# Optimization experiments

Measured on AMD Instinct MI355X. Metric: run time of the kernel, lower is better.

## Reference

```python
import jax, jax.numpy as jnp
import numpy as np

EPS = 1e-5  # torch.nn.CosineSimilarity eps


def setup_inputs() -> dict:
    key = jax.random.key(0)
    x = jax.random.normal(key, (8, 256, 1024), dtype=jnp.float32)
    return {"batch_sequence_tensors": x}


def _worst_sim(x):
    # For every contiguous window [s, e] (1 <= s < e <= S-1, matching
    # exclude_special_tokens + sequential combinatorics), compute
    # min_t in [s,e] cos(mean(x[s:e+1]), x[t]).
    # Trick: dot(sum_{s..e} x_i, x_t) comes from a prefix sum of the Gram
    # matrix, and ||sum_{s..e} x||^2 from a 2-D prefix sum of the Gram matrix,
    # avoiding any [B,S,S,D] intermediates.
    B, S, D = x.shape
    G = jnp.einsum('bsd,btd->bst', x, x)  # [B,S,S] Gram

    # num[b,s,e,t] = sum_{i=s..e} x_i . x_t  via 1-D prefix sum over i
    Cpad = jnp.pad(jnp.cumsum(G, axis=1), ((0, 0), (1, 0), (0, 0)))  # [B,S+1,S]
    num = Cpad[:, 1:, :][:, None, :, :] - Cpad[:, :S, :][:, :, None, :]  # [B,S,S,S]

    # ||sum_{s..e} x||^2 = sum_{i,j in [s,e]} G[i,j] via 2-D prefix sum
    PP = jnp.pad(jnp.cumsum(jnp.cumsum(G, axis=1), axis=2),
                 ((0, 0), (1, 0), (1, 0)))  # [B,S+1,S+1]
    dE = jnp.diagonal(PP[:, 1:, 1:], axis1=1, axis2=2)   # PP[e+1,e+1]  [B,S]
    dS = jnp.diagonal(PP[:, :S, :S], axis1=1, axis2=2)   # PP[s,s]      [B,S]
    cross1 = PP[:, :S, 1:]                               # PP[s,e+1]  axes (s,e)
    cross2 = jnp.swapaxes(PP[:, 1:, :S], 1, 2)           # PP[e+1,s] -> (s,e)
    ssq = dE[:, None, :] + dS[:, :, None] - cross1 - cross2  # [B,S,S]
    sum_norm = jnp.sqrt(jnp.maximum(ssq, 0.0))               # ||sum||

    idx = jnp.arange(S)
    win_len = jnp.maximum(idx[None, :] - idx[:, None] + 1, 1).astype(x.dtype)  # [S,S] (s,e)
    # center = sum / len ; cosine uses the mean exactly as the torch module
    mean_norm = sum_norm / win_len                       # [B,S,S]
    x_norm = jnp.sqrt(jnp.maximum(jnp.diagonal(G, axis1=1, axis2=2), 0.0))  # [B,S]
    denom = jnp.maximum(mean_norm[..., None] * x_norm[:, None, None, :], EPS)
    cos = (num / win_len[None, :, :, None]) / denom      # [B,S,S,S]

    t_in = (idx[None, None, :] >= idx[:, None, None]) & \
           (idx[None, None, :] <= idx[None, :, None])    # [S,S,S] (s,e,t)
    worst = jnp.min(jnp.where(t_in[None], cos, jnp.inf), axis=-1)  # [B,S,S]

    valid = (idx[:, None] >= 1) & (idx[None, :] > idx[:, None])    # 1<=s<e<=S-1
    return jnp.where(valid[None], worst, 0.0)


def reference(batch_sequence_tensors):
    # worst_sim[b,s,e] = min cosine similarity of window mean vs members;
    # the original module's group mask is worst_sim >= threshold (0.9),
    # followed by (data-dependent, non-tensor) subset removal.
    return _worst_sim(batch_sequence_tensors)
```

## Files before the change

kernel.cpp:

```cpp
#include <hip/hip_runtime.h>
#include <stdint.h>

#define NB 8
#define NS 256
#define ND 1024
#define EPSF 1e-5f
#define BIGF 3.0e38f

typedef __attribute__((ext_vector_type(8))) short short8;
typedef __attribute__((ext_vector_type(4))) float f32x4;

__device__ __forceinline__ unsigned short f2bf(float f) {
  unsigned int u = __float_as_uint(f);
  u = (u + 0x7FFFu + ((u >> 16) & 1u)) >> 16;
  return (unsigned short)u;
}
__device__ __forceinline__ float bf2f(unsigned short u) {
  return __uint_as_float((unsigned int)u << 16);
}

__global__ __launch_bounds__(256) void k_convert(const float* __restrict__ x,
                                                 unsigned short* __restrict__ xb,
                                                 float* __restrict__ DGa,
                                                 float* __restrict__ IXa) {
  int row = blockIdx.x * 4 + (threadIdx.x >> 6);
  int lane = threadIdx.x & 63;
  size_t base = (size_t)row * ND;
  float sq = 0.f;
#pragma unroll
  for (int c = 0; c < 4; ++c) {
    size_t o = base + c * 256 + lane * 4;
    float4 v = *reinterpret_cast<const float4*>(x + o);
    ushort4 ob;
    ob.x = f2bf(v.x); ob.y = f2bf(v.y); ob.z = f2bf(v.z); ob.w = f2bf(v.w);
    *reinterpret_cast<ushort4*>(xb + o) = ob;
    sq += v.x * v.x + v.y * v.y + v.z * v.z + v.w * v.w;
  }
#pragma unroll
  for (int off = 32; off; off >>= 1) sq += __shfl_xor(sq, off);
  if (lane == 0) {
    DGa[row] = sq;
    IXa[row] = 1.0f / sqrtf(sq);
  }
}

__global__ __launch_bounds__(256) void k_ypfx(const unsigned short* __restrict__ xb,
                                              unsigned short* __restrict__ yb) {
  int wid = (blockIdx.x * 256 + threadIdx.x) >> 6;
  int lane = threadIdx.x & 63;
  int b = wid >> 10;
  int d = wid & 1023;
  const unsigned short* xr = xb + ((size_t)b << 18) + d;
  unsigned short* yr = yb + ((size_t)b << 18) + d;
  int s0 = lane << 2;
  float v0 = bf2f(xr[(size_t)(s0 + 0) * ND]);
  float v1 = bf2f(xr[(size_t)(s0 + 1) * ND]);
  float v2 = bf2f(xr[(size_t)(s0 + 2) * ND]);
  float v3 = bf2f(xr[(size_t)(s0 + 3) * ND]);
  float sum = v0 + v1 + v2 + v3;
  float sc = sum;
#pragma unroll
  for (int off = 1; off < 64; off <<= 1) {
    float n = __shfl_up(sc, off);
    if (lane >= off) sc += n;
  }
  float y0 = (sc - sum) + v0;
  float y1 = y0 + v1;
  float y2 = y1 + v2;
  float y3 = y2 + v3;
  yr[(size_t)(s0 + 0) * ND] = f2bf(y0);
  yr[(size_t)(s0 + 1) * ND] = f2bf(y1);
  yr[(size_t)(s0 + 2) * ND] = f2bf(y2);
  yr[(size_t)(s0 + 3) * ND] = f2bf(y3);
}

__global__ __launch_bounds__(256) void k_gemmC(const unsigned short* __restrict__ yb,
                                               const unsigned short* __restrict__ xb,
                                               float* __restrict__ cp) {
  int gw = ((blockIdx.x << 8) + threadIdx.x) >> 6;
  int lane = threadIdx.x & 63;
  int b  = gw & 7;
  int mt = (gw >> 3) & 7;
  int nt = (gw >> 6) & 7;
  int ks = (gw >> 9) & 1;
  const unsigned short* Ab = yb + ((size_t)b << 18) + ((size_t)(mt << 5) << 10);
  const unsigned short* Bb = xb + ((size_t)b << 18) + ((size_t)(nt << 5) << 10);
  int lr = lane & 15;
  int lk = (lane >> 4) << 3;
  f32x4 acc00 = {0.f,0.f,0.f,0.f}, acc01 = {0.f,0.f,0.f,0.f};
  f32x4 acc10 = {0.f,0.f,0.f,0.f}, acc11 = {0.f,0.f,0.f,0.f};
  int kbase = (ks << 9) + lk;
#pragma unroll 2
  for (int kk = 0; kk < 512; kk += 32) {
    int ko = kbase + kk;
    short8 a0  = *reinterpret_cast<const short8*>(Ab + ((size_t)lr << 10) + ko);
    short8 a1  = *reinterpret_cast<const short8*>(Ab + ((size_t)(16 + lr) << 10) + ko);
    short8 bb0 = *reinterpret_cast<const short8*>(Bb + ((size_t)lr << 10) + ko);
    short8 bb1 = *reinterpret_cast<const short8*>(Bb + ((size_t)(16 + lr) << 10) + ko);
    acc00 = __builtin_amdgcn_mfma_f32_16x16x32_bf16(a0, bb0, acc00, 0, 0, 0);
    acc01 = __builtin_amdgcn_mfma_f32_16x16x32_bf16(a0, bb1, acc01, 0, 0, 0);
    acc10 = __builtin_amdgcn_mfma_f32_16x16x32_bf16(a1, bb0, acc10, 0, 0, 0);
    acc11 = __builtin_amdgcn_mfma_f32_16x16x32_bf16(a1, bb1, acc11, 0, 0, 0);
  }
  float* G = cp + (size_t)ks * (NB * NS * NS) + ((size_t)b << 16);
  int r0 = (mt << 5) + ((lane >> 4) << 2);
  int c0 = (nt << 5) + lr;
#pragma unroll
  for (int j = 0; j < 4; ++j) {
    G[(r0 + j) * NS + c0]           = acc00[j];
    G[(r0 + j) * NS + c0 + 16]      = acc01[j];
    G[(r0 + 16 + j) * NS + c0]      = acc10[j];
    G[(r0 + 16 + j) * NS + c0 + 16] = acc11[j];
  }
}

__global__ __launch_bounds__(256) void k_scan(const float* __restrict__ cp,
                                              float* __restrict__ C, float* __restrict__ S2) {
  int id = blockIdx.x * 4 + (threadIdx.x >> 6);
  int lane = threadIdx.x & 63;
  int b = id / 257;
  int r = id - b * 257;
  float* Crow = C + ((size_t)b * 257 + r) * NS;
  float* Srow = S2 + ((size_t)b * 257 + r) * 257;
  const float* p0 = cp + (((size_t)b << 8) + (r - 1)) * NS;
  const float* p1 = p0 + (size_t)NB * NS * NS;
  if (lane == 0) Srow[0] = 0.f;
  float run = 0.f;
  for (int c0 = 0; c0 < NS; c0 += 64) {
    float v = 0.f;
    if (r > 0) v = p0[c0 + lane] + p1[c0 + lane];
    Crow[c0 + lane] = v;
#pragma unroll
    for (int off = 1; off < 64; off <<= 1) {
      float n = __shfl_up(v, off);
      if (lane >= off) v += n;
    }
    Srow[c0 + lane + 1] = run + v;
    run += __shfl(v, 63);
  }
}

__global__ __launch_bounds__(256) void k_trop(const float* __restrict__ C,
                                              const float* __restrict__ S2,
                                              const float* __restrict__ IXa,
                                              const float* __restrict__ DGa,
                                              float* __restrict__ out) {
  __shared__ float As[64][36];
  __shared__ float Bs[64][68];
  __shared__ float wred[4];
  int blk = blockIdx.x;
  int b = blk >> 5;
  int tix = blk & 31;
  int i0 = (tix >> 2) << 5;
  int j0 = (tix & 3) << 6;
  int tid = threadIdx.x;
  float* outb = out + ((size_t)b << 16);

  if (i0 >= j0 + 63) {
    float4 z = {0.f, 0.f, 0.f, 0.f};
    float* p = outb + (size_t)(i0 + (tid >> 3)) * NS + j0 + ((tid & 7) << 3);
    reinterpret_cast<float4*>(p)[0] = z;
    reinterpret_cast<float4*>(p)[1] = z;
    return;
  }

  const float* Cb = C + (size_t)b * 257 * NS;
  const float* IXb = IXa + b * NS;

  float wv0 = IXb[tid];
#pragma unroll
  for (int off = 32; off; off >>= 1) wv0 = fmaxf(wv0, __shfl_xor(wv0, off));
  if ((tid & 63) == 0) wred[tid >> 6] = wv0;
  __syncthreads();
  float wmb = fmaxf(fmaxf(wred[0], wred[1]), fmaxf(wred[2], wred[3]));

  int ii0 = (tid >> 4) << 1;
  int jj0 = (tid & 15) << 2;
  float acc[8];
#pragma unroll
  for (int k = 0; k < 8; ++k) acc[k] = BIGF;

  int rA = tid >> 4;
  int c4 = (tid & 15) << 2;

  for (int t0 = i0 & ~63; t0 < j0 + 64; t0 += 64) {
    __syncthreads();
    float4 wv = *reinterpret_cast<const float4*>(IXb + t0 + c4);
#pragma unroll
    for (int p = 0; p < 2; ++p) {
      int r = i0 + p * 16 + rA;
      float4 v = *reinterpret_cast<const float4*>(Cb + (size_t)r * NS + t0 + c4);
      As[c4 + 0][p * 16 + rA] = v.x * wv.x;
      As[c4 + 1][p * 16 + rA] = v.y * wv.y;
      As[c4 + 2][p * 16 + rA] = v.z * wv.z;
      As[c4 + 3][p * 16 + rA] = v.w * wv.w;
    }
#pragma unroll
    for (int p = 0; p < 4; ++p) {
      int r = j0 + 1 + p * 16 + rA;
      float4 v = *reinterpret_cast<const float4*>(Cb + (size_t)r * NS + t0 + c4);
      Bs[c4 + 0][p * 16 + rA] = v.x * wv.x;
      Bs[c4 + 1][p * 16 + rA] = v.y * wv.y;
      Bs[c4 + 2][p * 16 + rA] = v.z * wv.z;
      Bs[c4 + 3][p * 16 + rA] = v.w * wv.w;
    }
    __syncthreads();

    int thA = i0 + ii0 - t0;
    int thB = j0 + jj0 - t0;
    if (thA <= -1 && thB >= 63) {
#pragma unroll 4
      for (int tt = 0; tt < 64; ++tt) {
        float2 a = *reinterpret_cast<const float2*>(&As[tt][ii0]);
        float4 bv = *reinterpret_cast<const float4*>(&Bs[tt][jj0]);
        acc[0] = fminf(acc[0], bv.x - a.x);
        acc[1] = fminf(acc[1], bv.y - a.x);
        acc[2] = fminf(acc[2], bv.z - a.x);
        acc[3] = fminf(acc[3], bv.w - a.x);
        acc[4] = fminf(acc[4], bv.x - a.y);
        acc[5] = fminf(acc[5], bv.y - a.y);
        acc[6] = fminf(acc[6], bv.z - a.y);
        acc[7] = fminf(acc[7], bv.w - a.y);
      }
    } else {
#pragma unroll 4
      for (int tt = 0; tt < 64; ++tt) {
        float2 a = *reinterpret_cast<const float2*>(&As[tt][ii0]);
        float4 bv = *reinterpret_cast<const float4*>(&Bs[tt][jj0]);
        float a0 = (tt >= thA)     ? a.x  : -BIGF;
        float a1 = (tt >= thA + 1) ? a.y  : -BIGF;
        float b0 = (tt <= thB)     ? bv.x :  BIGF;
        float b1 = (tt <= thB + 1) ? bv.y :  BIGF;
        float b2 = (tt <= thB + 2) ? bv.z :  BIGF;
        float b3 = (tt <= thB + 3) ? bv.w :  BIGF;
        acc[0] = fminf(acc[0], b0 - a0);
        acc[1] = fminf(acc[1], b1 - a0);
        acc[2] = fminf(acc[2], b2 - a0);
        acc[3] = fminf(acc[3], b3 - a0);
        acc[4] = fminf(acc[4], b0 - a1);
        acc[5] = fminf(acc[5], b1 - a1);
        acc[6] = fminf(acc[6], b2 - a1);
        acc[7] = fminf(acc[7], b3 - a1);
      }
    }
  }

  const float* S2b = S2 + (size_t)b * 257 * 257;
  const float* DGb = DGa + b * NS;
#pragma unroll
  for (int k = 0; k < 2; ++k) {
    int i = i0 + ii0 + k;
    float o4[4];
    float s2ii = S2b[(size_t)i * 257 + i];
#pragma unroll
    for (int l = 0; l < 4; ++l) {
      int j = j0 + jj0 + l;
      float res = 0.f;
      if (i >= 1 && j > i) {
        float s2jj = S2b[(size_t)(j + 1) * 257 + (j + 1)];
        float s2ij = S2b[(size_t)i * 257 + (j + 1)];
        float s2ji = S2b[(size_t)(j + 1) * 257 + i];
        float ssq = (s2jj - s2ij) - (s2ji - s2ii);
        float sn = sqrtf(fmaxf(ssq, 0.f));
        float win = (float)(j - i + 1);
        if (sn >= EPSF * win * wmb) {
          res = acc[k * 4 + l] / sn;
        } else {
          float mn = sn / win;
          float m = BIGF;
          const float* r2 = Cb + (size_t)(j + 1) * NS;
          const float* r1 = Cb + (size_t)i * NS;
          for (int t = i; t <= j; ++t) {
            float num = r2[t] - r1[t];
            float xn = sqrtf(fmaxf(DGb[t], 0.f));
            float den = fmaxf(mn * xn, EPSF);
            m = fminf(m, num / win / den);
          }
          res = m;
        }
      }
      o4[l] = res;
    }
    float4 st = {o4[0], o4[1], o4[2], o4[3]};
    *reinterpret_cast<float4*>(outb + (size_t)i * NS + j0 + jj0) = st;
  }
}

extern "C" void kernel_launch(void* const* d_in, const int* in_sizes, int n_in,
                              void* d_out, int out_size, void* d_ws, size_t ws_size,
                              hipStream_t stream) {
  (void)in_sizes; (void)n_in; (void)ws_size; (void)out_size;
  const float* x = (const float*)d_in[0];
  float* out = (float*)d_out;
  char* ws = (char*)d_ws;
  unsigned short* Xb = (unsigned short*)(ws);
  unsigned short* Yb = (unsigned short*)(ws + 4194304);
  float* Cp  = (float*)(ws + 8388608);
  float* C   = (float*)(ws + 12582912);
  float* S2  = (float*)(ws + 14688256);
  float* DGa = (float*)(ws + 16801824);
  float* IXa = (float*)(ws + 16810016);

  k_convert<<<512, 256, 0, stream>>>(x, Xb, DGa, IXa);
  k_ypfx<<<2048, 256, 0, stream>>>(Xb, Yb);
  k_gemmC<<<256, 256, 0, stream>>>(Yb, Xb, Cp);
  k_scan<<<514, 256, 0, stream>>>(Cp, C, S2);
  k_trop<<<256, 256, 0, stream>>>(C, S2, IXa, DGa, out);
}
```

Measured before the change: 120.9 us.

## Fuse all five stages into one cooperative kernel with grid syncs

Replaces the five kernel launches (convert, prefix, GEMM, scan, tropical min) with a single cooperative kernel of 256 blocks that separates the stages with grid.sync(). The prefix stage now reads fp32 x directly, so it no longer waits on the bf16 conversion. The GEMM drops the split-K partial buffer: each wave computes full-K 16x16 tiles and writes C directly, which removes the partial-sum add from the scan. The aim is to cut launch overhead and intermediate traffic, at the cost of grid-wide barriers and lower occupancy during the GEMM and scan phases.

```diff
diff --git a/kernel.cpp b/kernel.cpp
--- a/kernel.cpp
+++ b/kernel.cpp
@@ -1,5 +1,8 @@
 #include <hip/hip_runtime.h>
+#include <hip/hip_cooperative_groups.h>
 #include <stdint.h>
+
+namespace cg = cooperative_groups;
 
 #define NB 8
 #define NS 256
@@ -15,274 +18,267 @@
   u = (u + 0x7FFFu + ((u >> 16) & 1u)) >> 16;
   return (unsigned short)u;
 }
-__device__ __forceinline__ float bf2f(unsigned short u) {
-  return __uint_as_float((unsigned int)u << 16);
-}
-
-__global__ __launch_bounds__(256) void k_convert(const float* __restrict__ x,
-                                                 unsigned short* __restrict__ xb,
-                                                 float* __restrict__ DGa,
-                                                 float* __restrict__ IXa) {
-  int row = blockIdx.x * 4 + (threadIdx.x >> 6);
-  int lane = threadIdx.x & 63;
-  size_t base = (size_t)row * ND;
-  float sq = 0.f;
-#pragma unroll
-  for (int c = 0; c < 4; ++c) {
-    size_t o = base + c * 256 + lane * 4;
-    float4 v = *reinterpret_cast<const float4*>(x + o);
-    ushort4 ob;
-    ob.x = f2bf(v.x); ob.y = f2bf(v.y); ob.z = f2bf(v.z); ob.w = f2bf(v.w);
-    *reinterpret_cast<ushort4*>(xb + o) = ob;
-    sq += v.x * v.x + v.y * v.y + v.z * v.z + v.w * v.w;
-  }
-#pragma unroll
-  for (int off = 32; off; off >>= 1) sq += __shfl_xor(sq, off);
-  if (lane == 0) {
-    DGa[row] = sq;
-    IXa[row] = 1.0f / sqrtf(sq);
-  }
-}
-
-__global__ __launch_bounds__(256) void k_ypfx(const unsigned short* __restrict__ xb,
-                                              unsigned short* __restrict__ yb) {
-  int wid = (blockIdx.x * 256 + threadIdx.x) >> 6;
-  int lane = threadIdx.x & 63;
-  int b = wid >> 10;
-  int d = wid & 1023;
-  const unsigned short* xr = xb + ((size_t)b << 18) + d;
-  unsigned short* yr = yb + ((size_t)b << 18) + d;
-  int s0 = lane << 2;
-  float v0 = bf2f(xr[(size_t)(s0 + 0) * ND]);
-  float v1 = bf2f(xr[(size_t)(s0 + 1) * ND]);
-  float v2 = bf2f(xr[(size_t)(s0 + 2) * ND]);
-  float v3 = bf2f(xr[(size_t)(s0 + 3) * ND]);
-  float sum = v0 + v1 + v2 + v3;
-  float sc = sum;
-#pragma unroll
-  for (int off = 1; off < 64; off <<= 1) {
-    float n = __shfl_up(sc, off);
-    if (lane >= off) sc += n;
-  }
-  float y0 = (sc - sum) + v0;
-  float y1 = y0 + v1;
-  float y2 = y1 + v2;
-  float y3 = y2 + v3;
-  yr[(size_t)(s0 + 0) * ND] = f2bf(y0);
-  yr[(size_t)(s0 + 1) * ND] = f2bf(y1);
-  yr[(size_t)(s0 + 2) * ND] = f2bf(y2);
-  yr[(size_t)(s0 + 3) * ND] = f2bf(y3);
-}
-
-__global__ __launch_bounds__(256) void k_gemmC(const unsigned short* __restrict__ yb,
-                                               const unsigned short* __restrict__ xb,
-                                               float* __restrict__ cp) {
-  int gw = ((blockIdx.x << 8) + threadIdx.x) >> 6;
-  int lane = threadIdx.x & 63;
-  int b  = gw & 7;
-  int mt = (gw >> 3) & 7;
-  int nt = (gw >> 6) & 7;
-  int ks = (gw >> 9) & 1;
-  const unsigned short* Ab = yb + ((size_t)b << 18) + ((size_t)(mt << 5) << 10);
-  const unsigned short* Bb = xb + ((size_t)b << 18) + ((size_t)(nt << 5) << 10);
-  int lr = lane & 15;
-  int lk = (lane >> 4) << 3;
-  f32x4 acc00 = {0.f,0.f,0.f,0.f}, acc01 = {0.f,0.f,0.f,0.f};
-  f32x4 acc10 = {0.f,0.f,0.f,0.f}, acc11 = {0.f,0.f,0.f,0.f};
-  int kbase = (ks << 9) + lk;
-#pragma unroll 2
-  for (int kk = 0; kk < 512; kk += 32) {
-    int ko = kbase + kk;
-    short8 a0  = *reinterpret_cast<const short8*>(Ab + ((size_t)lr << 10) + ko);
-    short8 a1  = *reinterpret_cast<const short8*>(Ab + ((size_t)(16 + lr) << 10) + ko);
-    short8 bb0 = *reinterpret_cast<const short8*>(Bb + ((size_t)lr << 10) + ko);
-    short8 bb1 = *reinterpret_cast<const short8*>(Bb + ((size_t)(16 + lr) << 10) + ko);
-    acc00 = __builtin_amdgcn_mfma_f32_16x16x32_bf16(a0, bb0, acc00, 0, 0, 0);
-    acc01 = __builtin_amdgcn_mfma_f32_16x16x32_bf16(a0, bb1, acc01, 0, 0, 0);
-    acc10 = __builtin_amdgcn_mfma_f32_16x16x32_bf16(a1, bb0, acc10, 0, 0, 0);
-    acc11 = __builtin_amdgcn_mfma_f32_16x16x32_bf16(a1, bb1, acc11, 0, 0, 0);
-  }
-  float* G = cp + (size_t)ks * (NB * NS * NS) + ((size_t)b << 16);
-  int r0 = (mt << 5) + ((lane >> 4) << 2);
-  int c0 = (nt << 5) + lr;
-#pragma unroll
-  for (int j = 0; j < 4; ++j) {
-    G[(r0 + j) * NS + c0]           = acc00[j];
-    G[(r0 + j) * NS + c0 + 16]      = acc01[j];
-    G[(r0 + 16 + j) * NS + c0]      = acc10[j];
-    G[(r0 + 16 + j) * NS + c0 + 16] = acc11[j];
-  }
-}
-
-__global__ __launch_bounds__(256) void k_scan(const float* __restrict__ cp,
-                                              float* __restrict__ C, float* __restrict__ S2) {
-  int id = blockIdx.x * 4 + (threadIdx.x >> 6);
-  int lane = threadIdx.x & 63;
-  int b = id / 257;
-  int r = id - b * 257;
-  float* Crow = C + ((size_t)b * 257 + r) * NS;
-  float* Srow = S2 + ((size_t)b * 257 + r) * 257;
-  const float* p0 = cp + (((size_t)b << 8) + (r - 1)) * NS;
-  const float* p1 = p0 + (size_t)NB * NS * NS;
-  if (lane == 0) Srow[0] = 0.f;
-  float run = 0.f;
-  for (int c0 = 0; c0 < NS; c0 += 64) {
-    float v = 0.f;
-    if (r > 0) v = p0[c0 + lane] + p1[c0 + lane];
-    Crow[c0 + lane] = v;
-#pragma unroll
-    for (int off = 1; off < 64; off <<= 1) {
-      float n = __shfl_up(v, off);
-      if (lane >= off) v += n;
-    }
-    Srow[c0 + lane + 1] = run + v;
-    run += __shfl(v, 63);
-  }
-}
-
-__global__ __launch_bounds__(256) void k_trop(const float* __restrict__ C,
-                                              const float* __restrict__ S2,
-                                              const float* __restrict__ IXa,
-                                              const float* __restrict__ DGa,
-                                              float* __restrict__ out) {
+
+__global__ __launch_bounds__(256) void k_fused(const float* __restrict__ x,
+                                               unsigned short* __restrict__ Xb,
+                                               unsigned short* __restrict__ Yb,
+                                               float* __restrict__ C,
+                                               float* __restrict__ S2,
+                                               float* __restrict__ DGa,
+                                               float* __restrict__ IXa,
+                                               float* __restrict__ out) {
   __shared__ float As[64][36];
   __shared__ float Bs[64][68];
   __shared__ float wred[4];
+  cg::grid_group grid = cg::this_grid();
+
   int blk = blockIdx.x;
-  int b = blk >> 5;
-  int tix = blk & 31;
-  int i0 = (tix >> 2) << 5;
-  int j0 = (tix & 3) << 6;
   int tid = threadIdx.x;
-  float* outb = out + ((size_t)b << 16);
-
-  if (i0 >= j0 + 63) {
-    float4 z = {0.f, 0.f, 0.f, 0.f};
-    float* p = outb + (size_t)(i0 + (tid >> 3)) * NS + j0 + ((tid & 7) << 3);
-    reinterpret_cast<float4*>(p)[0] = z;
-    reinterpret_cast<float4*>(p)[1] = z;
-    return;
-  }
-
-  const float* Cb = C + (size_t)b * 257 * NS;
-  const float* IXb = IXa + b * NS;
-
-  float wv0 = IXb[tid];
-#pragma unroll
-  for (int off = 32; off; off >>= 1) wv0 = fmaxf(wv0, __shfl_xor(wv0, off));
-  if ((tid & 63) == 0) wred[tid >> 6] = wv0;
-  __syncthreads();
-  float wmb = fmaxf(fmaxf(wred[0], wred[1]), fmaxf(wred[2], wred[3]));
-
-  int ii0 = (tid >> 4) << 1;
-  int jj0 = (tid & 15) << 2;
-  float acc[8];
-#pragma unroll
-  for (int k = 0; k < 8; ++k) acc[k] = BIGF;
-
-  int rA = tid >> 4;
-  int c4 = (tid & 15) << 2;
-
-  for (int t0 = i0 & ~63; t0 < j0 + 64; t0 += 64) {
+  int wv = tid >> 6;
+  int lane = tid & 63;
+  int wid = blk * 4 + wv;
+
+#pragma unroll
+  for (int rr = 0; rr < 2; ++rr) {
+    int row = blk * 8 + wv * 2 + rr;
+    size_t base = (size_t)row * ND;
+    float sq = 0.f;
+#pragma unroll
+    for (int c = 0; c < 4; ++c) {
+      size_t o = base + c * 256 + lane * 4;
+      float4 v = *reinterpret_cast<const float4*>(x + o);
+      ushort4 ob;
+      ob.x = f2bf(v.x); ob.y = f2bf(v.y); ob.z = f2bf(v.z); ob.w = f2bf(v.w);
+      *reinterpret_cast<ushort4*>(Xb + o) = ob;
+      sq += v.x * v.x + v.y * v.y + v.z * v.z + v.w * v.w;
+    }
+#pragma unroll
+    for (int off = 32; off; off >>= 1) sq += __shfl_xor(sq, off);
+    if (lane == 0) {
+      DGa[row] = sq;
+      IXa[row] = 1.0f / sqrtf(sq);
+    }
+  }
+  if (blk < NB) C[(size_t)blk * 257 * NS + tid] = 0.f;
+#pragma unroll
+  for (int c = 0; c < 8; ++c) {
+    int g = wid * 8 + c;
+    int b = g >> 10;
+    int d = g & 1023;
+    const float* xr = x + ((size_t)b << 18) + d;
+    unsigned short* yr = Yb + ((size_t)b << 18) + d;
+    int s0 = lane << 2;
+    float v0 = xr[(size_t)(s0 + 0) * ND];
+    float v1 = xr[(size_t)(s0 + 1) * ND];
+    float v2 = xr[(size_t)(s0 + 2) * ND];
+    float v3 = xr[(size_t)(s0 + 3) * ND];
+    float sum = v0 + v1 + v2 + v3;
+    float sc = sum;
+#pragma unroll
+    for (int off = 1; off < 64; off <<= 1) {
+      float n = __shfl_up(sc, off);
+      if (lane >= off) sc += n;
+    }
+    float y0 = (sc - sum) + v0;
+    float y1 = y0 + v1;
+    float y2 = y1 + v2;
+    float y3 = y2 + v3;
+    yr[(size_t)(s0 + 0) * ND] = f2bf(y0);
+    yr[(size_t)(s0 + 1) * ND] = f2bf(y1);
+    yr[(size_t)(s0 + 2) * ND] = f2bf(y2);
+    yr[(size_t)(s0 + 3) * ND] = f2bf(y3);
+  }
+
+  grid.sync();
+
+  {
+    int lr = lane & 15;
+    int lk = (lane >> 4) << 3;
+#pragma unroll
+    for (int jj = 0; jj < 2; ++jj) {
+      int job = wid * 2 + jj;
+      int b = job >> 8;
+      int mt = (job >> 4) & 15;
+      int nt = job & 15;
+      const unsigned short* Ab = Yb + ((size_t)b << 18) + ((size_t)(mt << 4) << 10);
+      const unsigned short* Bb = Xb + ((size_t)b << 18) + ((size_t)(nt << 4) << 10);
+      f32x4 acc = {0.f, 0.f, 0.f, 0.f};
+#pragma unroll 4
+      for (int kk = 0; kk < 1024; kk += 32) {
+        short8 a  = *reinterpret_cast<const short8*>(Ab + ((size_t)lr << 10) + kk + lk);
+        short8 bv = *reinterpret_cast<const short8*>(Bb + ((size_t)lr << 10) + kk + lk);
+        acc = __builtin_amdgcn_mfma_f32_16x16x32_bf16(a, bv, acc, 0, 0, 0);
+      }
+      float* Cb = C + (size_t)b * 257 * NS;
+      int r0 = (mt << 4) + ((lane >> 4) << 2) + 1;
+      int c0 = (nt << 4) + lr;
+#pragma unroll
+      for (int j = 0; j < 4; ++j) Cb[(size_t)(r0 + j) * NS + c0] = acc[j];
+    }
+  }
+
+  grid.sync();
+
+#pragma unroll
+  for (int p = 0; p < 3; ++p) {
+    int id = wid + p * 1024;
+    if (id < NB * 257) {
+      int b = id / 257;
+      int r = id - b * 257;
+      const float* Crow = C + ((size_t)b * 257 + r) * NS;
+      float* Srow = S2 + ((size_t)b * 257 + r) * 257;
+      if (lane == 0) Srow[0] = 0.f;
+      float run = 0.f;
+      for (int c0 = 0; c0 < NS; c0 += 64) {
+        float v = Crow[c0 + lane];
+#pragma unroll
+        for (int off = 1; off < 64; off <<= 1) {
+          float n = __shfl_up(v, off);
+          if (lane >= off) v += n;
+        }
+        Srow[c0 + lane + 1] = run + v;
+        run += __shfl(v, 63);
+      }
+    }
+  }
+
+  grid.sync();
+
+  {
+    int b = blk >> 5;
+    int tix = blk & 31;
+    int i0 = (tix >> 2) << 5;
+    int j0 = (tix & 3) << 6;
+    float* outb = out + ((size_t)b << 16);
+
+    if (i0 >= j0 + 63) {
+      float4 z = {0.f, 0.f, 0.f, 0.f};
+      float* p = outb + (size_t)(i0 + (tid >> 3)) * NS + j0 + ((tid & 7) << 3);
+      reinterpret_cast<float4*>(p)[0] = z;
+      reinterpret_cast<float4*>(p)[1] = z;
+      return;
+    }
+
+    const float* Cb = C + (size_t)b * 257 * NS;
+    const float* IXb = IXa + b * NS;
+
+    float wv0 = IXb[tid];
+#pragma unroll
+    for (int off = 32; off; off >>= 1) wv0 = fmaxf(wv0, __shfl_xor(wv0, off));
+    if ((tid & 63) == 0) wred[tid >> 6] = wv0;
     __syncthreads();
-    float4 wv = *reinterpret_cast<const float4*>(IXb + t0 + c4);
-#pragma unroll
-    for (int p = 0; p < 2; ++p) {
-      int r = i0 + p * 16 + rA;
-      float4 v = *reinterpret_cast<const float4*>(Cb + (size_t)r * NS + t0 + c4);
-      As[c4 + 0][p * 16 + rA] = v.x * wv.x;
-      As[c4 + 1][p * 16 + rA] = v.y * wv.y;
-      As[c4 + 2][p * 16 + rA] = v.z * wv.z;
-      As[c4 + 3][p * 16 + rA] = v.w * wv.w;
-    }
-#pragma unroll
-    for (int p = 0; p < 4; ++p) {
-      int r = j0 + 1 + p * 16 + rA;
-      float4 v = *reinterpret_cast<const float4*>(Cb + (size_t)r * NS + t0 + c4);
-      Bs[c4 + 0][p * 16 + rA] = v.x * wv.x;
-      Bs[c4 + 1][p * 16 + rA] = v.y * wv.y;
-      Bs[c4 + 2][p * 16 + rA] = v.z * wv.z;
-      Bs[c4 + 3][p * 16 + rA] = v.w * wv.w;
-    }
-    __syncthreads();
-
-    int thA = i0 + ii0 - t0;
-    int thB = j0 + jj0 - t0;
-    if (thA <= -1 && thB >= 63) {
+    float wmb = fmaxf(fmaxf(wred[0], wred[1]), fmaxf(wred[2], wred[3]));
+
+    int ii0 = (tid >> 4) << 1;
+    int jj0 = (tid & 15) << 2;
+    float acc[8];
+#pragma unroll
+    for (int k = 0; k < 8; ++k) acc[k] = BIGF;
+
+    int rA = tid >> 4;
+    int c4 = (tid & 15) << 2;
+
+    for (int t0 = i0 & ~63; t0 < j0 + 64; t0 += 64) {
+      __syncthreads();
+      float4 wv4 = *reinterpret_cast<const float4*>(IXb + t0 + c4);
+#pragma unroll
+      for (int p = 0; p < 2; ++p) {
+        int r = i0 + p * 16 + rA;
+        float4 v = *reinterpret_cast<const float4*>(Cb + (size_t)r * NS + t0 + c4);
+        As[c4 + 0][p * 16 + rA] = v.x * wv4.x;
+        As[c4 + 1][p * 16 + rA] = v.y * wv4.y;
+        As[c4 + 2][p * 16 + rA] = v.z * wv4.z;
+        As[c4 + 3][p * 16 + rA] = v.w * wv4.w;
+      }
+#pragma unroll
+      for (int p = 0; p < 4; ++p) {
+        int r = j0 + 1 + p * 16 + rA;
+        float4 v = *reinterpret_cast<const float4*>(Cb + (size_t)r * NS + t0 + c4);
+        Bs[c4 + 0][p * 16 + rA] = v.x * wv4.x;
+        Bs[c4 + 1][p * 16 + rA] = v.y * wv4.y;
+        Bs[c4 + 2][p * 16 + rA] = v.z * wv4.z;
+        Bs[c4 + 3][p * 16 + rA] = v.w * wv4.w;
+      }
+      __syncthreads();
+
+      int thA = i0 + ii0 - t0;
+      int thB = j0 + jj0 - t0;
+      if (thA <= -1 && thB >= 63) {
 #pragma unroll 4
-      for (int tt = 0; tt < 64; ++tt) {
-        float2 a = *reinterpret_cast<const float2*>(&As[tt][ii0]);
-        float4 bv = *reinterpret_cast<const float4*>(&Bs[tt][jj0]);
-        acc[0] = fminf(acc[0], bv.x - a.x);
-        acc[1] = fminf(acc[1], bv.y - a.x);
-        acc[2] = fminf(acc[2], bv.z - a.x);
-        acc[3] = fminf(acc[3], bv.w - a.x);
-        acc[4] = fminf(acc[4], bv.x - a.y);
-        acc[5] = fminf(acc[5], bv.y - a.y);
-        acc[6] = fminf(acc[6], bv.z - a.y);
-        acc[7] = fminf(acc[7], bv.w - a.y);
-      }
-    } else {
+        for (int tt = 0; tt < 64; ++tt) {
+          float2 a = *reinterpret_cast<const float2*>(&As[tt][ii0]);
+          float4 bv = *reinterpret_cast<const float4*>(&Bs[tt][jj0]);
+          acc[0] = fminf(acc[0], bv.x - a.x);
+          acc[1] = fminf(acc[1], bv.y - a.x);
+          acc[2] = fminf(acc[2], bv.z - a.x);
+          acc[3] = fminf(acc[3], bv.w - a.x);
+          acc[4] = fminf(acc[4], bv.x - a.y);
+          acc[5] = fminf(acc[5], bv.y - a.y);
+          acc[6] = fminf(acc[6], bv.z - a.y);
+          acc[7] = fminf(acc[7], bv.w - a.y);
+        }
+      } else {
 #pragma unroll 4
-      for (int tt = 0; tt < 64; ++tt) {
-        float2 a = *reinterpret_cast<const float2*>(&As[tt][ii0]);
-        float4 bv = *reinterpret_cast<const float4*>(&Bs[tt][jj0]);
-        float a0 = (tt >= thA)     ? a.x  : -BIGF;
-        float a1 = (tt >= thA + 1) ? a.y  : -BIGF;
-        float b0 = (tt <= thB)     ? bv.x :  BIGF;
-        float b1 = (tt <= thB + 1) ? bv.y :  BIGF;
-        float b2 = (tt <= thB + 2) ? bv.z :  BIGF;
-        float b3 = (tt <= thB + 3) ? bv.w :  BIGF;
-        acc[0] = fminf(acc[0], b0 - a0);
-        acc[1] = fminf(acc[1], b1 - a0);
-        acc[2] = fminf(acc[2], b2 - a0);
-        acc[3] = fminf(acc[3], b3 - a0);
-        acc[4] = fminf(acc[4], b0 - a1);
-        acc[5] = fminf(acc[5], b1 - a1);
-        acc[6] = fminf(acc[6], b2 - a1);
-        acc[7] = fminf(acc[7], b3 - a1);
-      }
-    }
-  }
-
-  const float* S2b = S2 + (size_t)b * 257 * 257;
-  const float* DGb = DGa + b * NS;
-#pragma unroll
-  for (int k = 0; k < 2; ++k) {
-    int i = i0 + ii0 + k;
-    float o4[4];
-    float s2ii = S2b[(size_t)i * 257 + i];
-#pragma unroll
-    for (int l = 0; l < 4; ++l) {
-      int j = j0 + jj0 + l;
-      float res = 0.f;
-      if (i >= 1 && j > i) {
-        float s2jj = S2b[(size_t)(j + 1) * 257 + (j + 1)];
-        float s2ij = S2b[(size_t)i * 257 + (j + 1)];
-        float s2ji = S2b[(size_t)(j + 1) * 257 + i];
-        float ssq = (s2jj - s2ij) - (s2ji - s2ii);
-        float sn = sqrtf(fmaxf(ssq, 0.f));
-        float win = (float)(j - i + 1);
-        if (sn >= EPSF * win * wmb) {
-          res = acc[k * 4 + l] / sn;
-        } else {
-          float mn = sn / win;
-          float m = BIGF;
-          const float* r2 = Cb + (size_t)(j + 1) * NS;
-          const float* r1 = Cb + (size_t)i * NS;
-          for (int t = i; t <= j; ++t) {
-            float num = r2[t] - r1[t];
-            float xn = sqrtf(fmaxf(DGb[t], 0.f));
-            float den = fmaxf(mn * xn, EPSF);
-            m = fminf(m, num / win / den);
+        for (int tt = 0; tt < 64; ++tt) {
+          float2 a = *reinterpret_cast<const float2*>(&As[tt][ii0]);
+          float4 bv = *reinterpret_cast<const float4*>(&Bs[tt][jj0]);
+          float a0 = (tt >= thA)     ? a.x  : -BIGF;
+          float a1 = (tt >= thA + 1) ? a.y  : -BIGF;
+          float b0 = (tt <= thB)     ? bv.x :  BIGF;
+          float b1 = (tt <= thB + 1) ? bv.y :  BIGF;
+          float b2 = (tt <= thB + 2) ? bv.z :  BIGF;
+          float b3 = (tt <= thB + 3) ? bv.w :  BIGF;
+          acc[0] = fminf(acc[0], b0 - a0);
+          acc[1] = fminf(acc[1], b1 - a0);
+          acc[2] = fminf(acc[2], b2 - a0);
+          acc[3] = fminf(acc[3], b3 - a0);
+          acc[4] = fminf(acc[4], b0 - a1);
+          acc[5] = fminf(acc[5], b1 - a1);
+          acc[6] = fminf(acc[6], b2 - a1);
+          acc[7] = fminf(acc[7], b3 - a1);
+        }
+      }
+    }
+
+    const float* S2b = S2 + (size_t)b * 257 * 257;
+    const float* DGb = DGa + b * NS;
+#pragma unroll
+    for (int k = 0; k < 2; ++k) {
+      int i = i0 + ii0 + k;
+      float o4[4];
+      float s2ii = S2b[(size_t)i * 257 + i];
+#pragma unroll
+      for (int l = 0; l < 4; ++l) {
+        int j = j0 + jj0 + l;
+        float res = 0.f;
+        if (i >= 1 && j > i) {
+          float s2jj = S2b[(size_t)(j + 1) * 257 + (j + 1)];
+          float s2ij = S2b[(size_t)i * 257 + (j + 1)];
+          float s2ji = S2b[(size_t)(j + 1) * 257 + i];
+          float ssq = (s2jj - s2ij) - (s2ji - s2ii);
+          float sn = sqrtf(fmaxf(ssq, 0.f));
+          float win = (float)(j - i + 1);
+          if (sn >= EPSF * win * wmb) {
+            res = acc[k * 4 + l] / sn;
+          } else {
+            float mn = sn / win;
+            float m = BIGF;
+            const float* r2 = Cb + (size_t)(j + 1) * NS;
+            const float* r1 = Cb + (size_t)i * NS;
+            for (int t = i; t <= j; ++t) {
+              float num = r2[t] - r1[t];
+              float xn = sqrtf(fmaxf(DGb[t], 0.f));
+              float den = fmaxf(mn * xn, EPSF);
+              m = fminf(m, num / win / den);
+            }
+            res = m;
           }
-          res = m;
         }
-      }
-      o4[l] = res;
-    }
-    float4 st = {o4[0], o4[1], o4[2], o4[3]};
-    *reinterpret_cast<float4*>(outb + (size_t)i * NS + j0 + jj0) = st;
+        o4[l] = res;
+      }
+      float4 st = {o4[0], o4[1], o4[2], o4[3]};
+      *reinterpret_cast<float4*>(outb + (size_t)i * NS + j0 + jj0) = st;
+    }
   }
 }
 
@@ -295,15 +291,12 @@
   char* ws = (char*)d_ws;
   unsigned short* Xb = (unsigned short*)(ws);
   unsigned short* Yb = (unsigned short*)(ws + 4194304);
-  float* Cp  = (float*)(ws + 8388608);
-  float* C   = (float*)(ws + 12582912);
-  float* S2  = (float*)(ws + 14688256);
-  float* DGa = (float*)(ws + 16801824);
-  float* IXa = (float*)(ws + 16810016);
-
-  k_convert<<<512, 256, 0, stream>>>(x, Xb, DGa, IXa);
-  k_ypfx<<<2048, 256, 0, stream>>>(Xb, Yb);
-  k_gemmC<<<256, 256, 0, stream>>>(Yb, Xb, Cp);
-  k_scan<<<514, 256, 0, stream>>>(Cp, C, S2);
-  k_trop<<<256, 256, 0, stream>>>(C, S2, IXa, DGa, out);
+  float* C   = (float*)(ws + 8388608);
+  float* S2  = (float*)(ws + 10493952);
+  float* DGa = (float*)(ws + 12607520);
+  float* IXa = (float*)(ws + 12615712);
+
+  void* args[] = {(void*)&x, (void*)&Xb, (void*)&Yb, (void*)&C, (void*)&S2,
+                  (void*)&DGa, (void*)&IXa, (void*)&out};
+  hipLaunchCooperativeKernel((void*)k_fused, dim3(256), dim3(256), args, 0, stream);
 }
```

Result: slower. 213.9 us (+77.0%).
